# Kernel tuning notes

Measured on AMD Instinct MI355X. Metric: run time of the kernel, lower is better.

The kernel has to match this reference:

```python
import jax, jax.numpy as jnp
import numpy as np

B = 16      # number of point clouds
N = 4096    # points per cloud (max segment size, static)
D = 3       # xyz


def setup_inputs() -> dict:
    key = jax.random.key(0)
    k1, k2 = jax.random.split(key)
    pred = jax.random.normal(k1, (B * N, D), dtype=jnp.float32)
    target = jax.random.normal(k2, (B * N, D), dtype=jnp.float32)
    # sorted batch assignment with equal-size segments (so N_max is static)
    batch = jnp.repeat(jnp.arange(B, dtype=jnp.int64), N)
    return {"pred": pred, "target": target, "batch": batch}


def _to_dense_batch(x, batch):
    # Faithful to torch_geometric.utils.to_dense_batch: scatter each point into
    # its (cloud, within-cloud-position) slot; padding slots stay zero.
    T = x.shape[0]
    counts = jax.ops.segment_sum(jnp.ones((T,), jnp.int32), batch, num_segments=B)
    starts = jnp.concatenate([jnp.zeros((1,), jnp.int32), jnp.cumsum(counts)[:-1]])
    pos = jnp.arange(T, dtype=jnp.int32) - starts[batch]
    dense = jnp.zeros((B, N, x.shape[1]), x.dtype).at[batch, pos].set(x)
    return dense


def _chamfer(x, y):
    # pytorch3d.loss.chamfer_distance defaults: squared L2, point_reduction="mean",
    # batch_reduction="mean"; no lengths -> padded zeros count as points (as in source).
    x2 = jnp.sum(x * x, axis=-1)                      # [B, N]
    y2 = jnp.sum(y * y, axis=-1)                      # [B, N]
    xy = jnp.einsum("bid,bjd->bij", x, y)             # [B, N, N]
    d2 = x2[:, :, None] + y2[:, None, :] - 2.0 * xy   # [B, N, N] squared dists
    cham_x = jnp.mean(jnp.min(d2, axis=2), axis=1)    # x -> nearest y, mean over points
    cham_y = jnp.mean(jnp.min(d2, axis=1), axis=1)    # y -> nearest x
    return jnp.mean(cham_x + cham_y)                  # batch mean of summed directions


def reference(pred, target, batch):
    dense_x = _to_dense_batch(pred, batch)
    dense_y = _to_dense_batch(target, batch)
    return _chamfer(dense_x, dense_y)
```

## Files before the change

### kernel.cpp

```cpp
#include <hip/hip_runtime.h>


typedef __attribute__((ext_vector_type(8))) short bf16x8;
typedef __attribute__((ext_vector_type(16))) float floatx16;

#define BB 16
#define NN 4096
#define T  256
#define NW 4
#define RS 2
#define XC (NW * RS * 32)
#define YB 512
#define YT 32
#define NT (YB / YT)
#define NXB (NN / XC)
#define NYB (NN / YB)
#define ONEBF 0x3F80u

__device__ __forceinline__ unsigned int f2bf(float f) {
    unsigned int u = __float_as_uint(f);
    u += 0x7fffu + ((u >> 16) & 1u);
    return u >> 16;
}
__device__ __forceinline__ float bf2f(unsigned int h) {
    return __uint_as_float(h << 16);
}
__device__ __forceinline__ float tree16(const floatx16& d) {
    float t0 = fminf(fminf(d[0], d[1]), d[2]);
    float t1 = fminf(fminf(d[3], d[4]), d[5]);
    float t2 = fminf(fminf(d[6], d[7]), d[8]);
    float t3 = fminf(fminf(d[9], d[10]), d[11]);
    float t4 = fminf(fminf(d[12], d[13]), d[14]);
    float u0 = fminf(fminf(t0, t1), t2);
    float u1 = fminf(fminf(t3, t4), d[15]);
    return fminf(u0, u1);
}

__global__ __launch_bounds__(T, 2) void chamfer_mfma(
    const float* __restrict__ pred,
    const float* __restrict__ target,
    float* __restrict__ rowp,
    float* __restrict__ colf)
{
    __shared__ uint4 ldsy[2][YB];
    __shared__ float colp[NW * YB];

    const int xb    = blockIdx.x;
    const int b     = blockIdx.y;
    const int yb    = blockIdx.z;
    const int xbase = xb * XC;
    const int ybase = yb * YB;
    const float* prd = pred   + (size_t)b * NN * 3;
    const float* tgt = target + (size_t)b * NN * 3;
    const int tid  = threadIdx.x;
    const int lane = tid & 63, w = tid >> 6;
    const int kg   = lane >> 5, m = lane & 31;

    for (int yl = tid; yl < YB; yl += T) {
        const float* yp = tgt + (size_t)(ybase + yl) * 3;
        float y0 = yp[0], y1 = yp[1], y2 = yp[2];
        unsigned int h0 = f2bf(y0), h1 = f2bf(y1), h2 = f2bf(y2);
        unsigned int H0 = f2bf(-2.f * bf2f(h0));
        unsigned int H1 = f2bf(-2.f * bf2f(h1));
        unsigned int H2 = f2bf(-2.f * bf2f(h2));
        unsigned int L0 = f2bf(-2.f * (y0 - bf2f(h0)));
        unsigned int L1 = f2bf(-2.f * (y1 - bf2f(h1)));
        unsigned int L2 = f2bf(-2.f * (y2 - bf2f(h2)));
        float ysq = fmaf(y0, y0, fmaf(y1, y1, y2 * y2));
        unsigned int sh = f2bf(ysq);
        unsigned int sl = f2bf(ysq - bf2f(sh));
        ldsy[0][yl] = make_uint4(H0 | (H1 << 16), H2 | (H0 << 16),
                                 H1 | (H2 << 16), L0 | (L1 << 16));
        ldsy[1][yl] = make_uint4(L2 | (ONEBF << 16), ONEBF | (sh << 16),
                                 sl, 0u);
    }

    unsigned int av[RS][4];
#pragma unroll
    for (int s = 0; s < RS; ++s) {
        int xi = xbase + w * (RS * 32) + s * 32 + m;
        const float* xp = prd + (size_t)xi * 3;
        float x0 = xp[0], x1 = xp[1], x2 = xp[2];
        unsigned int h0 = f2bf(x0), h1 = f2bf(x1), h2 = f2bf(x2);
        unsigned int L0 = f2bf(x0 - bf2f(h0));
        unsigned int L1 = f2bf(x1 - bf2f(h1));
        unsigned int L2 = f2bf(x2 - bf2f(h2));
        float xsq = fmaf(x0, x0, fmaf(x1, x1, x2 * x2));
        unsigned int sh = f2bf(xsq);
        unsigned int sl = f2bf(xsq - bf2f(sh));
        av[s][0] = kg ? (h2 | (sh << 16))    : (h0 | (h1 << 16));
        av[s][1] = kg ? (sl | (ONEBF << 16)) : (h2 | (L0 << 16));
        av[s][2] = kg ? ONEBF                : (L1 | (L2 << 16));
        av[s][3] = kg ? 0u                   : (h0 | (h1 << 16));
    }
    __syncthreads();

    floatx16 acc[RS];
#pragma unroll
    for (int s = 0; s < RS; ++s)
#pragma unroll
        for (int r = 0; r < 16; ++r) acc[s][r] = 3.402823466e38f;
    floatx16 zacc;
#pragma unroll
    for (int r = 0; r < 16; ++r) zacc[r] = 0.f;

    union U { uint4 q; bf16x8 v; };
    uint4 bc0 = ldsy[kg][m];
    uint4 bc1 = ldsy[kg][YT + m];
    for (int t = 0; t < NT; t += 2) {
        int tn = (t + 2 < NT) ? t + 2 : 0;
        uint4 bn0 = ldsy[kg][tn * YT + m];
        uint4 bn1 = ldsy[kg][(tn + 1) * YT + m];
        U bu0; bu0.q = bc0;
        U bu1; bu1.q = bc1;
        float cp0 = 3.402823466e38f, cp1 = 3.402823466e38f;
#pragma unroll
        for (int s = 0; s < RS; ++s) {
            U au; au.q = make_uint4(av[s][0], av[s][1], av[s][2], av[s][3]);
            floatx16 d0 = __builtin_amdgcn_mfma_f32_32x32x16_bf16(
                au.v, bu0.v, zacc, 0, 0, 0);
            floatx16 d1 = __builtin_amdgcn_mfma_f32_32x32x16_bf16(
                au.v, bu1.v, zacc, 0, 0, 0);
#pragma unroll
            for (int r = 0; r < 16; ++r)
                acc[s][r] = fminf(fminf(acc[s][r], d0[r]), d1[r]);
            cp0 = fminf(cp0, tree16(d0));
            cp1 = fminf(cp1, tree16(d1));
        }
        cp0 = fminf(cp0, __shfl_xor(cp0, 32, 64));
        cp1 = fminf(cp1, __shfl_xor(cp1, 32, 64));
        if (kg == 0) {
            colp[w * YB + t * YT + m]       = cp0;
            colp[w * YB + (t + 1) * YT + m] = cp1;
        }
        bc0 = bn0; bc1 = bn1;
    }

    float* rowbase = rowp + ((size_t)(b * NXB + xb) * NYB + yb) * XC;
#pragma unroll
    for (int s = 0; s < RS; ++s) {
#pragma unroll
        for (int r = 0; r < 16; ++r) {
            float v = acc[s][r];
            v = fminf(v, __shfl_xor(v, 1, 64));
            v = fminf(v, __shfl_xor(v, 2, 64));
            v = fminf(v, __shfl_xor(v, 4, 64));
            v = fminf(v, __shfl_xor(v, 8, 64));
            v = fminf(v, __shfl_xor(v, 16, 64));
            if (m == 0) {
                int row = (r & 3) + 8 * (r >> 2) + 4 * kg;
                rowbase[w * (RS * 32) + s * 32 + row] = v;
            }
        }
    }

    __syncthreads();
    float* colbase = colf + ((size_t)(b * NYB + yb) * NXB + xb) * YB;
    for (int yl = tid; yl < YB; yl += T) {
        float v = fminf(fminf(colp[yl], colp[YB + yl]),
                        fminf(colp[2 * YB + yl], colp[3 * YB + yl]));
        colbase[yl] = v;
    }
}

__global__ __launch_bounds__(256) void chamfer_reduce2(
    const float* __restrict__ rowp, const float* __restrict__ colf,
    float* __restrict__ out)
{
    int e = blockIdx.x * 256 + threadIdx.x;
    float v = 3.402823466e38f;
    if (e < BB * NN) {
        int b = e >> 12, xi = e & (NN - 1);
        int xb = xi >> 8, li = xi & (XC - 1);
        const float* p = rowp + ((size_t)(b * NXB + xb) * NYB) * XC + li;
#pragma unroll
        for (int yb = 0; yb < NYB; ++yb) v = fminf(v, p[yb * XC]);
    } else {
        int f = e - BB * NN;
        int b = f >> 12, y = f & (NN - 1);
        int yb = y >> 9, yl = y & (YB - 1);
        const float* p = colf + ((size_t)(b * NYB + yb) * NXB) * YB + yl;
#pragma unroll
        for (int xb = 0; xb < NXB; ++xb) v = fminf(v, p[xb * YB]);
    }
    float s = fmaxf(v, 0.f);
#pragma unroll
    for (int off = 32; off > 0; off >>= 1)
        s += __shfl_down(s, off, 64);
    __shared__ float wsum[4];
    if ((threadIdx.x & 63) == 0) wsum[threadIdx.x >> 6] = s;
    __syncthreads();
    if (threadIdx.x == 0) {
        float t = wsum[0] + wsum[1] + wsum[2] + wsum[3];
        atomicAdd(out, t * (1.0f / (BB * NN)));
    }
}

extern "C" void kernel_launch(void* const* d_in, const int* in_sizes, int n_in,
                              void* d_out, int out_size, void* d_ws, size_t ws_size,
                              hipStream_t stream) {
    const float* pred   = (const float*)d_in[0];
    const float* target = (const float*)d_in[1];
    float* out  = (float*)d_out;
    float* rowp = (float*)d_ws;
    float* colf = rowp + (size_t)BB * NXB * NYB * XC;

    hipMemsetAsync(out, 0, sizeof(float), stream);
    dim3 grid(NXB, BB, NYB);
    chamfer_mfma<<<grid, T, 0, stream>>>(pred, target, rowp, colf);
    chamfer_reduce2<<<512, 256, 0, stream>>>(rowp, colf, out);
}
```

Baseline: 94.97 us.

## Precompute target bf16 records in a prep kernel and halve x-tile per block

Moves the per-block conversion of target points into split-bf16 MFMA operands into a separate prep kernel that writes packed records to workspace, so each main block only copies them into LDS. The x tile per block shrinks from 256 to 128 rows (one 32-row slab per wave), which doubles the grid and lowers register pressure, but it also doubles the number of target tile loads and the column-partial traffic. The software prefetch of B operands is dropped in favour of direct LDS reads with unroll 2. An extra kernel launch is added, and the final reduction reads twice as many column partials.

```diff
diff --git a/kernel.cpp b/kernel.cpp
--- a/kernel.cpp
+++ b/kernel.cpp
@@ -7,14 +7,13 @@
 #define BB 16
 #define NN 4096
 #define T  256
-#define NW 4
-#define RS 2
-#define XC (NW * RS * 32)
+#define NPTS (BB * NN)
+#define XC 128
+#define NXB (NN / XC)
 #define YB 512
+#define NYB (NN / YB)
 #define YT 32
 #define NT (YB / YT)
-#define NXB (NN / XC)
-#define NYB (NN / YB)
 #define ONEBF 0x3F80u
 
 __device__ __forceinline__ unsigned int f2bf(float f) {
@@ -36,50 +35,56 @@
     return fminf(u0, u1);
 }
 
-__global__ __launch_bounds__(T, 2) void chamfer_mfma(
+__global__ __launch_bounds__(T) void chamfer_prep(
+    const float* __restrict__ target,
+    uint4* __restrict__ rec0, uint4* __restrict__ rec1)
+{
+    int g = blockIdx.x * T + threadIdx.x;
+    const float* yp = target + (size_t)g * 3;
+    float y0 = yp[0], y1 = yp[1], y2 = yp[2];
+    unsigned int h0 = f2bf(y0), h1 = f2bf(y1), h2 = f2bf(y2);
+    unsigned int H0 = f2bf(-2.f * bf2f(h0));
+    unsigned int H1 = f2bf(-2.f * bf2f(h1));
+    unsigned int H2 = f2bf(-2.f * bf2f(h2));
+    unsigned int L0 = f2bf(-2.f * (y0 - bf2f(h0)));
+    unsigned int L1 = f2bf(-2.f * (y1 - bf2f(h1)));
+    unsigned int L2 = f2bf(-2.f * (y2 - bf2f(h2)));
+    float ysq = fmaf(y0, y0, fmaf(y1, y1, y2 * y2));
+    unsigned int sh = f2bf(ysq);
+    unsigned int sl = f2bf(ysq - bf2f(sh));
+    rec0[g] = make_uint4(H0 | (H1 << 16), H2 | (H0 << 16),
+                         H1 | (H2 << 16), L0 | (L1 << 16));
+    rec1[g] = make_uint4(L2 | (ONEBF << 16), ONEBF | (sh << 16),
+                         sl, 0u);
+}
+
+__global__ __launch_bounds__(T, 2) void chamfer_main(
     const float* __restrict__ pred,
-    const float* __restrict__ target,
+    const uint4* __restrict__ rec0, const uint4* __restrict__ rec1,
     float* __restrict__ rowp,
     float* __restrict__ colf)
 {
     __shared__ uint4 ldsy[2][YB];
-    __shared__ float colp[NW * YB];
-
-    const int xb    = blockIdx.x;
-    const int b     = blockIdx.y;
-    const int yb    = blockIdx.z;
-    const int xbase = xb * XC;
-    const int ybase = yb * YB;
-    const float* prd = pred   + (size_t)b * NN * 3;
-    const float* tgt = target + (size_t)b * NN * 3;
+    __shared__ float colp[4][YB];
+
+    const int xb = blockIdx.x;
+    const int b  = blockIdx.y;
+    const int yb = blockIdx.z;
+    const size_t ygbase = (size_t)b * NN + (size_t)yb * YB;
     const int tid  = threadIdx.x;
     const int lane = tid & 63, w = tid >> 6;
     const int kg   = lane >> 5, m = lane & 31;
 
-    for (int yl = tid; yl < YB; yl += T) {
-        const float* yp = tgt + (size_t)(ybase + yl) * 3;
-        float y0 = yp[0], y1 = yp[1], y2 = yp[2];
-        unsigned int h0 = f2bf(y0), h1 = f2bf(y1), h2 = f2bf(y2);
-        unsigned int H0 = f2bf(-2.f * bf2f(h0));
-        unsigned int H1 = f2bf(-2.f * bf2f(h1));
-        unsigned int H2 = f2bf(-2.f * bf2f(h2));
-        unsigned int L0 = f2bf(-2.f * (y0 - bf2f(h0)));
-        unsigned int L1 = f2bf(-2.f * (y1 - bf2f(h1)));
-        unsigned int L2 = f2bf(-2.f * (y2 - bf2f(h2)));
-        float ysq = fmaf(y0, y0, fmaf(y1, y1, y2 * y2));
-        unsigned int sh = f2bf(ysq);
-        unsigned int sl = f2bf(ysq - bf2f(sh));
-        ldsy[0][yl] = make_uint4(H0 | (H1 << 16), H2 | (H0 << 16),
-                                 H1 | (H2 << 16), L0 | (L1 << 16));
-        ldsy[1][yl] = make_uint4(L2 | (ONEBF << 16), ONEBF | (sh << 16),
-                                 sl, 0u);
-    }
-
-    unsigned int av[RS][4];
-#pragma unroll
-    for (int s = 0; s < RS; ++s) {
-        int xi = xbase + w * (RS * 32) + s * 32 + m;
-        const float* xp = prd + (size_t)xi * 3;
+    for (int i = tid; i < YB; i += T) {
+        ldsy[0][i] = rec0[ygbase + i];
+        ldsy[1][i] = rec1[ygbase + i];
+    }
+
+    union U { uint4 q; bf16x8 v; };
+    U au;
+    {
+        int xi = b * NN + xb * XC + w * 32 + m;
+        const float* xp = pred + (size_t)xi * 3;
         float x0 = xp[0], x1 = xp[1], x2 = xp[2];
         unsigned int h0 = f2bf(x0), h1 = f2bf(x1), h2 = f2bf(x2);
         unsigned int L0 = f2bf(x0 - bf2f(h0));
@@ -88,95 +93,75 @@
         float xsq = fmaf(x0, x0, fmaf(x1, x1, x2 * x2));
         unsigned int sh = f2bf(xsq);
         unsigned int sl = f2bf(xsq - bf2f(sh));
-        av[s][0] = kg ? (h2 | (sh << 16))    : (h0 | (h1 << 16));
-        av[s][1] = kg ? (sl | (ONEBF << 16)) : (h2 | (L0 << 16));
-        av[s][2] = kg ? ONEBF                : (L1 | (L2 << 16));
-        av[s][3] = kg ? 0u                   : (h0 | (h1 << 16));
-    }
+        au.q = make_uint4(kg ? (h2 | (sh << 16))    : (h0 | (h1 << 16)),
+                          kg ? (sl | (ONEBF << 16)) : (h2 | (L0 << 16)),
+                          kg ? ONEBF                : (L1 | (L2 << 16)),
+                          kg ? 0u                   : (h0 | (h1 << 16)));
+    }
+
+    floatx16 acc, zacc;
+#pragma unroll
+    for (int r = 0; r < 16; ++r) { acc[r] = 3.402823466e38f; zacc[r] = 0.f; }
     __syncthreads();
 
-    floatx16 acc[RS];
-#pragma unroll
-    for (int s = 0; s < RS; ++s)
-#pragma unroll
-        for (int r = 0; r < 16; ++r) acc[s][r] = 3.402823466e38f;
-    floatx16 zacc;
-#pragma unroll
-    for (int r = 0; r < 16; ++r) zacc[r] = 0.f;
-
-    union U { uint4 q; bf16x8 v; };
-    uint4 bc0 = ldsy[kg][m];
-    uint4 bc1 = ldsy[kg][YT + m];
+#pragma unroll 2
     for (int t = 0; t < NT; t += 2) {
-        int tn = (t + 2 < NT) ? t + 2 : 0;
-        uint4 bn0 = ldsy[kg][tn * YT + m];
-        uint4 bn1 = ldsy[kg][(tn + 1) * YT + m];
-        U bu0; bu0.q = bc0;
-        U bu1; bu1.q = bc1;
-        float cp0 = 3.402823466e38f, cp1 = 3.402823466e38f;
-#pragma unroll
-        for (int s = 0; s < RS; ++s) {
-            U au; au.q = make_uint4(av[s][0], av[s][1], av[s][2], av[s][3]);
-            floatx16 d0 = __builtin_amdgcn_mfma_f32_32x32x16_bf16(
-                au.v, bu0.v, zacc, 0, 0, 0);
-            floatx16 d1 = __builtin_amdgcn_mfma_f32_32x32x16_bf16(
-                au.v, bu1.v, zacc, 0, 0, 0);
-#pragma unroll
-            for (int r = 0; r < 16; ++r)
-                acc[s][r] = fminf(fminf(acc[s][r], d0[r]), d1[r]);
-            cp0 = fminf(cp0, tree16(d0));
-            cp1 = fminf(cp1, tree16(d1));
-        }
+        U bu0, bu1;
+        bu0.q = ldsy[kg][t * YT + m];
+        bu1.q = ldsy[kg][(t + 1) * YT + m];
+        floatx16 d0 = __builtin_amdgcn_mfma_f32_32x32x16_bf16(
+            au.v, bu0.v, zacc, 0, 0, 0);
+        floatx16 d1 = __builtin_amdgcn_mfma_f32_32x32x16_bf16(
+            au.v, bu1.v, zacc, 0, 0, 0);
+#pragma unroll
+        for (int r = 0; r < 16; ++r)
+            acc[r] = fminf(fminf(acc[r], d0[r]), d1[r]);
+        float cp0 = tree16(d0);
+        float cp1 = tree16(d1);
         cp0 = fminf(cp0, __shfl_xor(cp0, 32, 64));
         cp1 = fminf(cp1, __shfl_xor(cp1, 32, 64));
         if (kg == 0) {
-            colp[w * YB + t * YT + m]       = cp0;
-            colp[w * YB + (t + 1) * YT + m] = cp1;
+            colp[w][t * YT + m]       = cp0;
+            colp[w][(t + 1) * YT + m] = cp1;
         }
-        bc0 = bn0; bc1 = bn1;
     }
 
     float* rowbase = rowp + ((size_t)(b * NXB + xb) * NYB + yb) * XC;
 #pragma unroll
-    for (int s = 0; s < RS; ++s) {
-#pragma unroll
-        for (int r = 0; r < 16; ++r) {
-            float v = acc[s][r];
-            v = fminf(v, __shfl_xor(v, 1, 64));
-            v = fminf(v, __shfl_xor(v, 2, 64));
-            v = fminf(v, __shfl_xor(v, 4, 64));
-            v = fminf(v, __shfl_xor(v, 8, 64));
-            v = fminf(v, __shfl_xor(v, 16, 64));
-            if (m == 0) {
-                int row = (r & 3) + 8 * (r >> 2) + 4 * kg;
-                rowbase[w * (RS * 32) + s * 32 + row] = v;
-            }
+    for (int r = 0; r < 16; ++r) {
+        float v = acc[r];
+        v = fminf(v, __shfl_xor(v, 1, 64));
+        v = fminf(v, __shfl_xor(v, 2, 64));
+        v = fminf(v, __shfl_xor(v, 4, 64));
+        v = fminf(v, __shfl_xor(v, 8, 64));
+        v = fminf(v, __shfl_xor(v, 16, 64));
+        if (m == 0) {
+            int row = (r & 3) + 8 * (r >> 2) + 4 * kg;
+            rowbase[w * 32 + row] = v;
         }
     }
 
     __syncthreads();
     float* colbase = colf + ((size_t)(b * NYB + yb) * NXB + xb) * YB;
-    for (int yl = tid; yl < YB; yl += T) {
-        float v = fminf(fminf(colp[yl], colp[YB + yl]),
-                        fminf(colp[2 * YB + yl], colp[3 * YB + yl]));
-        colbase[yl] = v;
-    }
-}
-
-__global__ __launch_bounds__(256) void chamfer_reduce2(
+    for (int yl = tid; yl < YB; yl += T)
+        colbase[yl] = fminf(fminf(colp[0][yl], colp[1][yl]),
+                            fminf(colp[2][yl], colp[3][yl]));
+}
+
+__global__ __launch_bounds__(T) void chamfer_final(
     const float* __restrict__ rowp, const float* __restrict__ colf,
     float* __restrict__ out)
 {
-    int e = blockIdx.x * 256 + threadIdx.x;
+    int e = blockIdx.x * T + threadIdx.x;
     float v = 3.402823466e38f;
-    if (e < BB * NN) {
+    if (e < NPTS) {
         int b = e >> 12, xi = e & (NN - 1);
-        int xb = xi >> 8, li = xi & (XC - 1);
+        int xb = xi >> 7, li = xi & (XC - 1);
         const float* p = rowp + ((size_t)(b * NXB + xb) * NYB) * XC + li;
 #pragma unroll
         for (int yb = 0; yb < NYB; ++yb) v = fminf(v, p[yb * XC]);
     } else {
-        int f = e - BB * NN;
+        int f = e - NPTS;
         int b = f >> 12, y = f & (NN - 1);
         int yb = y >> 9, yl = y & (YB - 1);
         const float* p = colf + ((size_t)(b * NYB + yb) * NXB) * YB + yl;
@@ -202,11 +187,14 @@
     const float* pred   = (const float*)d_in[0];
     const float* target = (const float*)d_in[1];
     float* out  = (float*)d_out;
-    float* rowp = (float*)d_ws;
+    uint4* rec0 = (uint4*)d_ws;
+    uint4* rec1 = rec0 + NPTS;
+    float* rowp = (float*)(rec1 + NPTS);
     float* colf = rowp + (size_t)BB * NXB * NYB * XC;
 
     hipMemsetAsync(out, 0, sizeof(float), stream);
+    chamfer_prep<<<NPTS / T, T, 0, stream>>>(target, rec0, rec1);
     dim3 grid(NXB, BB, NYB);
-    chamfer_mfma<<<grid, T, 0, stream>>>(pred, target, rowp, colf);
-    chamfer_reduce2<<<512, 256, 0, stream>>>(rowp, colf, out);
-}
+    chamfer_main<<<grid, T, 0, stream>>>(pred, rec0, rec1, rowp, colf);
+    chamfer_final<<<2 * NPTS / T, T, 0, stream>>>(rowp, colf, out);
+}
```

Result: slower. 103.1 us (+8.5%).
